# Performance work log

Measured on AMD Instinct MI355X. Metric: run time of the kernel, lower is better.

The kernel has to match this reference:

```python
import jax, jax.numpy as jnp
import numpy as np

B, Q, K, D = 32, 1024, 1024, 128

def setup_inputs() -> dict:
    key = jax.random.key(0)
    kq, kk, kv, kl = jax.random.split(key, 4)
    return {
        "queries": jax.random.normal(kq, (B, Q, D), dtype=jnp.float32),
        "keys": jax.random.normal(kk, (B, K, D), dtype=jnp.float32),
        "values": jax.random.normal(kv, (B, K, D), dtype=jnp.float32),
        "valid_length": jax.random.randint(kl, (B,), 1, K + 1),
    }

def reference(queries, keys, values, valid_length):
    d = queries.shape[-1]
    # scores: [B, Q, K]
    scores = jnp.einsum("bqd,bkd->bqk", queries, keys) / jnp.sqrt(jnp.float32(d))
    # length mask: position k is valid iff k < valid_length[b]
    mask = jnp.arange(keys.shape[1])[None, None, :] < valid_length[:, None, None]
    scores = jnp.where(mask, scores, jnp.float32(-1e9))
    attn = jax.nn.softmax(scores, axis=-1)
    # dropout module is identity in eval / p=0
    return jnp.einsum("bqk,bkv->bqv", attn, values)
```

## Files before the change

kernel.cpp:

```cpp
#include <hip/hip_runtime.h>
#include <hip/hip_bf16.h>
#include <stdint.h>

#define B_    32
#define QLEN  1024
#define KSEQ  1024
#define DIM   128
#define NKT   (KSEQ / 64)
#define SCALE 0.08838834764831845f
#define KSC   0.12751879522655792f

typedef __attribute__((ext_vector_type(8)))  short short8;
typedef __attribute__((ext_vector_type(4)))  float floatx4;
typedef __attribute__((ext_vector_type(16))) float floatx16;
typedef unsigned int u32;

__device__ __forceinline__ u32 f2bf(float x) {
  union { float f; u32 u; } v; v.f = x;
  return (v.u + 0x7FFF + ((v.u >> 16) & 1)) >> 16;
}
__device__ __forceinline__ u32 pack2(float lo, float hi) {
  return f2bf(lo) | (f2bf(hi) << 16);
}
__device__ __forceinline__ u32 cvtpk(float lo, float hi) {
  u32 d;
  asm("v_cvt_pk_bf16_f32 %0, %1, %2" : "=v"(d) : "v"(lo), "v"(hi));
  return d;
}
__device__ __forceinline__ void swap32(u32& a, u32& b) {
  asm volatile("v_permlane32_swap_b32 %0, %1" : "+v"(a), "+v"(b));
}
__device__ __forceinline__ float exp2_fast(float x) {
  float d;
  asm("v_exp_f32 %0, %1" : "=v"(d) : "v"(x));
  return d;
}
typedef union { uint4 u; short8 s; } U8;

__global__ __launch_bounds__(256) void prep_kernel(const float* __restrict__ Kg,
                                                   const float* __restrict__ Vg,
                                                   const int* __restrict__ vlen,
                                                   uint4* __restrict__ Ksw,
                                                   uint4* __restrict__ Vsw,
                                                   int2* __restrict__ task) {
  __shared__ __align__(16) u32 Vu[64 * 65];
  __shared__ __align__(16) uint4 Ku[64 * 17];
  __shared__ int sidx[32];
  const int kt = blockIdx.x, b = blockIdx.y, t = threadIdx.x;
  const bool tableblk = (blockIdx.z == 0) && (kt == 0) && (b == 0);

  if (tableblk && t < 64) {
    const int bb = t & 31;
    const int ntb = (vlen[bb] + 63) >> 6;
    int rank = 0;
#pragma unroll
    for (int j = 0; j < 32; j++) {
      const int ntj = __shfl(ntb, j);
      rank += (ntj > ntb) | ((ntj == ntb) & (j < bb));
    }
    if (t < 32) sidx[rank] = bb;
  }

  if (kt * 64 < vlen[b]) {
    if (blockIdx.z == 0) {
      const float* src = Kg + ((size_t)b * KSEQ + kt * 64) * DIM;
#pragma unroll
      for (int it = 0; it < 4; it++) {
        const int f = it * 256 + t, r = f >> 4, c = f & 15;
        floatx4 f0 = *(const floatx4*)(src + r * DIM + c * 8);
        floatx4 f1 = *(const floatx4*)(src + r * DIM + c * 8 + 4);
        uint4 o;
        o.x = pack2(f0[0] * KSC, f0[1] * KSC); o.y = pack2(f0[2] * KSC, f0[3] * KSC);
        o.z = pack2(f1[0] * KSC, f1[1] * KSC); o.w = pack2(f1[2] * KSC, f1[3] * KSC);
        Ku[r * 17 + c] = o;
      }
      __syncthreads();
      uint4* dst = Ksw + ((size_t)b * NKT + kt) * 1024;
#pragma unroll
      for (int it = 0; it < 4; it++) {
        const int o16 = it * 256 + t;
        const int kh = o16 >> 9, cs = (o16 >> 6) & 7, lane = o16 & 63;
        const int hi = lane >> 5, l31 = lane & 31;
        const int r = kh * 32 + l31, j = 2 * cs + hi;
        dst[o16] = Ku[r * 17 + j];
      }
    } else {
      const float* src = Vg + ((size_t)b * KSEQ + kt * 64) * DIM;
#pragma unroll
      for (int it = 0; it < 8; it++) {
        const int k = it * 8 + (t >> 5), c = t & 31;
        const floatx4 f = *(const floatx4*)(src + (size_t)k * DIM + c * 4);
        const int s = (k >> 3) & 4;
        Vu[k * 65 + ((2 * c) ^ s)]     = pack2(f[0], f[1]);
        Vu[k * 65 + ((2 * c + 1) ^ s)] = pack2(f[2], f[3]);
      }
      __syncthreads();
      uint4* dst = Vsw + ((size_t)b * NKT + kt) * 1024;
#pragma unroll
      for (int it = 0; it < 4; it++) {
        const int o16 = it * 256 + t;
        const int kh = o16 >> 9, slot = (o16 >> 6) & 7, lane = o16 & 63;
        const int dt = slot >> 1, i_ = slot & 1;
        const int hi = lane >> 5, l31 = lane & 31;
        const int d = dt * 32 + l31, m7 = d & 7;
        const int kc = (kh * 4 + 2 * i_ + hi);
        const int col = (d >> 1) ^ (kc & 4);
        u32 r[8];
#pragma unroll
        for (int j = 0; j < 8; j++) r[j] = Vu[(kc * 8 + j) * 65 + col];
        const u32 sel = (d & 1) ? 0x07060302u : 0x05040100u;
        uint4 o;
        o.x = __builtin_amdgcn_perm(r[1], r[0], sel);
        o.y = __builtin_amdgcn_perm(r[3], r[2], sel);
        o.z = __builtin_amdgcn_perm(r[5], r[4], sel);
        o.w = __builtin_amdgcn_perm(r[7], r[6], sel);
        dst[o16] = o;
      }
    }
  }

  if (tableblk) {
    __syncthreads();
    for (int l = t; l < 512; l += 256) {
      const int x = l & 7, j = l >> 3;
      int rank, q;
      if (j < 32) { rank = (j & 1) ? x + 8  : x;      q = j >> 1; }
      else        { rank = (j & 1) ? x + 16 : x + 24; q = (j - 32) >> 1; }
      task[l] = make_int2(sidx[rank], q << 6);
    }
  }
}

__global__ __launch_bounds__(256, 2) void attn_kernel(
    const float* __restrict__ Qg, const uint4* __restrict__ Ksw,
    const uint4* __restrict__ Vsw, const int* __restrict__ vlen,
    const int2* __restrict__ task, float* __restrict__ Og) {
  __shared__ float scr[64 * 128];
  __shared__ float Lred[2][32];

  const int2 tq = task[blockIdx.x];
  const int b = tq.x, q0 = tq.y;
  const int t = threadIdx.x, wave = t >> 6, lane = t & 63;
  const int qh = wave & 1, kh = wave >> 1;
  const int l31 = lane & 31, hi = lane >> 5;
  const int L  = vlen[b];
  const int nt = (L + 63) >> 6;

  const short* KtS = (const short*)(Ksw + (size_t)b * NKT * 1024) +
                     kh * 4096 + lane * 8;
  const short* Vt  = (const short*)(Vsw + (size_t)b * NKT * 1024) +
                     kh * 4096 + lane * 8;

  short8 qb[8];
  {
    const float* qrow = Qg + ((size_t)b * QLEN + q0 + qh * 32 + l31) * DIM;
#pragma unroll
    for (int c = 0; c < 8; c++) {
      floatx4 f0 = *(const floatx4*)(qrow + c * 16 + hi * 8);
      floatx4 f1 = *(const floatx4*)(qrow + c * 16 + hi * 8 + 4);
      short8 a;
      a[0] = (short)f2bf(f0[0]); a[1] = (short)f2bf(f0[1]);
      a[2] = (short)f2bf(f0[2]); a[3] = (short)f2bf(f0[3]);
      a[4] = (short)f2bf(f1[0]); a[5] = (short)f2bf(f1[1]);
      a[6] = (short)f2bf(f1[2]); a[7] = (short)f2bf(f1[3]);
      qb[c] = a;
    }
  }

  float lrow = 0.0f;
  floatx16 oacc[4];
#pragma unroll
  for (int dt = 0; dt < 4; dt++)
#pragma unroll
    for (int i = 0; i < 16; i++) oacc[dt][i] = 0.0f;

#define LOAD_K(DST, tkv)                                                       \
  {                                                                            \
    const short* kp_ = KtS + (size_t)(tkv) * 8192;                             \
    _Pragma("unroll") for (int c_ = 0; c_ < 8; c_++)                           \
      DST[c_] = *(const short8*)(kp_ + c_ * 512);                              \
  }

#define BODY(KF, tkv)                                                          \
  {                                                                            \
    const int k0_ = (tkv) * 64;                                                \
    short8 vb[4][2];                                                           \
    {                                                                          \
      const short* vt_ = Vt + (size_t)(tkv) * 8192;                            \
      _Pragma("unroll") for (int dt = 0; dt < 4; dt++) {                       \
        vb[dt][0] = *(const short8*)(vt_ + (dt * 2 + 0) * 512);                \
        vb[dt][1] = *(const short8*)(vt_ + (dt * 2 + 1) * 512);                \
      }                                                                        \
    }                                                                          \
    floatx16 s;                                                                \
    _Pragma("unroll") for (int i = 0; i < 16; i++) s[i] = 0.0f;                \
    __builtin_amdgcn_s_setprio(1);                                             \
    _Pragma("unroll") for (int c = 0; c < 8; c++)                              \
      s = __builtin_amdgcn_mfma_f32_32x32x16_bf16(KF[c], qb[c], s, 0, 0, 0);   \
    __builtin_amdgcn_s_setprio(0);                                             \
    if (k0_ + kh * 32 + 32 <= L) {                                             \
      _Pragma("unroll") for (int r = 0; r < 16; r++) {                         \
        s[r] = exp2_fast(s[r]);                                                \
        lrow += s[r];                                                          \
      }                                                                        \
    } else {                                                                   \
      _Pragma("unroll") for (int r = 0; r < 16; r++) {                         \
        const int ck = (r & 3) + 8 * (r >> 2) + 4 * hi;                        \
        const float a = (k0_ + kh * 32 + ck < L) ? exp2_fast(s[r]) : 0.0f;     \
        s[r] = a;                                                              \
        lrow += a;                                                             \
      }                                                                        \
    }                                                                          \
    {                                                                          \
      u32 u0 = cvtpk(s[0], s[1]),   u1 = cvtpk(s[2], s[3]);                    \
      u32 u2 = cvtpk(s[4], s[5]),   u3 = cvtpk(s[6], s[7]);                    \
      swap32(u0, u2); swap32(u1, u3);                                          \
      u32 w0 = cvtpk(s[8], s[9]),   w1 = cvtpk(s[10], s[11]);                  \
      u32 w2 = cvtpk(s[12], s[13]), w3 = cvtpk(s[14], s[15]);                  \
      swap32(w0, w2); swap32(w1, w3);                                          \
      U8 pu0; pu0.u.x = u0; pu0.u.y = u1; pu0.u.z = u2; pu0.u.w = u3;          \
      U8 pu1; pu1.u.x = w0; pu1.u.y = w1; pu1.u.z = w2; pu1.u.w = w3;          \
      __builtin_amdgcn_s_setprio(1);                                           \
      _Pragma("unroll") for (int dt = 0; dt < 4; dt++) {                       \
        oacc[dt] = __builtin_amdgcn_mfma_f32_32x32x16_bf16(pu0.s, vb[dt][0],   \
                                                           oacc[dt], 0, 0, 0);\
        oacc[dt] = __builtin_amdgcn_mfma_f32_32x32x16_bf16(pu1.s, vb[dt][1],   \
                                                           oacc[dt], 0, 0, 0);\
      }                                                                        \
      __builtin_amdgcn_s_setprio(0);                                           \
    }                                                                          \
  }

  short8 ka[8], kb[8];
  LOAD_K(ka, 0);
  int tk = 0;
  for (;;) {
    if (tk + 1 < nt) LOAD_K(kb, tk + 1);
    BODY(ka, tk);
    if (++tk == nt) break;
    if (tk + 1 < nt) LOAD_K(ka, tk + 1);
    BODY(kb, tk);
    if (++tk == nt) break;
  }

  lrow += __shfl_xor(lrow, 32);
  if (kh == 1) {
    if (lane < 32) Lred[qh][l31] = lrow;
#pragma unroll
    for (int dt = 0; dt < 4; dt++)
#pragma unroll
      for (int r = 0; r < 16; r++)
        scr[(dt * 16 + r) * 128 + qh * 64 + lane] = oacc[dt][r];
  }
  __syncthreads();
  if (kh == 0) {
    const float ltot = lrow + Lred[qh][l31];
    const float inv_ = 1.0f / ltot;
    float iv[16];
#pragma unroll
    for (int r = 0; r < 16; r++)
      iv[r] = __shfl(inv_, (r & 3) + 8 * (r >> 2) + 4 * hi);
    float* obase = Og + ((size_t)b * QLEN + q0 + qh * 32) * DIM + l31;
#pragma unroll
    for (int dt = 0; dt < 4; dt++) {
#pragma unroll
      for (int r = 0; r < 16; r++) {
        const int rq = (r & 3) + 8 * (r >> 2) + 4 * hi;
        const float v = oacc[dt][r] + scr[(dt * 16 + r) * 128 + qh * 64 + lane];
        obase[(size_t)rq * DIM + dt * 32] = v * iv[r];
      }
    }
  }
#undef LOAD_K
#undef BODY
}

extern "C" void kernel_launch(void* const* d_in, const int* in_sizes, int n_in,
                              void* d_out, int out_size, void* d_ws, size_t ws_size,
                              hipStream_t stream) {
  const float* Qg = (const float*)d_in[0];
  const float* Kg = (const float*)d_in[1];
  const float* Vg = (const float*)d_in[2];
  const int*  vln = (const int*)d_in[3];
  uint4* Ksw = (uint4*)d_ws;
  uint4* Vsw = (uint4*)((char*)d_ws + (size_t)B_ * NKT * 16384);
  int2*  Tsk = (int2*)((char*)d_ws + 2 * (size_t)B_ * NKT * 16384);

  prep_kernel<<<dim3(NKT, B_, 2), 256, 0, stream>>>(Kg, Vg, vln, Ksw, Vsw, Tsk);
  attn_kernel<<<dim3(512), 256, 0, stream>>>(Qg, Ksw, Vsw, vln, Tsk,
                                             (float*)d_out);
}
```

Baseline: 110.8 us.

## Software-pipeline QK^T of next tile with softmax and PV of current tile

Restructures the main loop so the QK^T MFMAs for tile k+1 are issued before the exp/convert/PV work of tile k, using two score accumulators (sA/sB) and a single K fragment buffer loaded two tiles ahead. The aim is to overlap matrix-core work with the transcendental and pack VALU work, and to hide K/V load latency. The row-sum is also turned into a tree reduction. The cost is extra register pressure from a second live 16-float score tile, which could lower occupancy or cause spills.

```diff
diff --git a/kernel.cpp b/kernel.cpp
--- a/kernel.cpp
+++ b/kernel.cpp
@@ -7,7 +7,6 @@
 #define KSEQ  1024
 #define DIM   128
 #define NKT   (KSEQ / 64)
-#define SCALE 0.08838834764831845f
 #define KSC   0.12751879522655792f
 
 typedef __attribute__((ext_vector_type(8)))  short short8;
@@ -102,7 +101,7 @@
         const int kh = o16 >> 9, slot = (o16 >> 6) & 7, lane = o16 & 63;
         const int dt = slot >> 1, i_ = slot & 1;
         const int hi = lane >> 5, l31 = lane & 31;
-        const int d = dt * 32 + l31, m7 = d & 7;
+        const int d = dt * 32 + l31;
         const int kc = (kh * 4 + 2 * i_ + hi);
         const int col = (d >> 1) ^ (kc & 4);
         u32 r[8];
@@ -174,72 +173,80 @@
 #pragma unroll
     for (int i = 0; i < 16; i++) oacc[dt][i] = 0.0f;
 
-#define LOAD_K(DST, tkv)                                                       \
+  short8 kf[8];
+  short8 vb[4][2];
+  floatx16 sA, sB;
+
+#define LOAD_K(tkv)                                                            \
   {                                                                            \
     const short* kp_ = KtS + (size_t)(tkv) * 8192;                             \
     _Pragma("unroll") for (int c_ = 0; c_ < 8; c_++)                           \
-      DST[c_] = *(const short8*)(kp_ + c_ * 512);                              \
-  }
-
-#define BODY(KF, tkv)                                                          \
+      kf[c_] = *(const short8*)(kp_ + c_ * 512);                               \
+  }
+
+#define LOAD_V(tkv)                                                            \
+  {                                                                            \
+    const short* vt_ = Vt + (size_t)(tkv) * 8192;                              \
+    _Pragma("unroll") for (int dt = 0; dt < 4; dt++) {                         \
+      vb[dt][0] = *(const short8*)(vt_ + (dt * 2 + 0) * 512);                  \
+      vb[dt][1] = *(const short8*)(vt_ + (dt * 2 + 1) * 512);                  \
+    }                                                                          \
+  }
+
+#define QKT(SD)                                                                \
+  {                                                                            \
+    _Pragma("unroll") for (int i = 0; i < 16; i++) SD[i] = 0.0f;               \
+    _Pragma("unroll") for (int c = 0; c < 8; c++)                              \
+      SD = __builtin_amdgcn_mfma_f32_32x32x16_bf16(kf[c], qb[c], SD, 0, 0, 0); \
+  }
+
+#define SMPV(SV, tkv)                                                          \
   {                                                                            \
     const int k0_ = (tkv) * 64;                                                \
-    short8 vb[4][2];                                                           \
-    {                                                                          \
-      const short* vt_ = Vt + (size_t)(tkv) * 8192;                            \
-      _Pragma("unroll") for (int dt = 0; dt < 4; dt++) {                       \
-        vb[dt][0] = *(const short8*)(vt_ + (dt * 2 + 0) * 512);                \
-        vb[dt][1] = *(const short8*)(vt_ + (dt * 2 + 1) * 512);                \
-      }                                                                        \
-    }                                                                          \
-    floatx16 s;                                                                \
-    _Pragma("unroll") for (int i = 0; i < 16; i++) s[i] = 0.0f;                \
-    __builtin_amdgcn_s_setprio(1);                                             \
-    _Pragma("unroll") for (int c = 0; c < 8; c++)                              \
-      s = __builtin_amdgcn_mfma_f32_32x32x16_bf16(KF[c], qb[c], s, 0, 0, 0);   \
-    __builtin_amdgcn_s_setprio(0);                                             \
     if (k0_ + kh * 32 + 32 <= L) {                                             \
-      _Pragma("unroll") for (int r = 0; r < 16; r++) {                         \
-        s[r] = exp2_fast(s[r]);                                                \
-        lrow += s[r];                                                          \
-      }                                                                        \
+      _Pragma("unroll") for (int r = 0; r < 16; r++) SV[r] = exp2_fast(SV[r]); \
     } else {                                                                   \
       _Pragma("unroll") for (int r = 0; r < 16; r++) {                         \
         const int ck = (r & 3) + 8 * (r >> 2) + 4 * hi;                        \
-        const float a = (k0_ + kh * 32 + ck < L) ? exp2_fast(s[r]) : 0.0f;     \
-        s[r] = a;                                                              \
-        lrow += a;                                                             \
+        SV[r] = (k0_ + kh * 32 + ck < L) ? exp2_fast(SV[r]) : 0.0f;            \
       }                                                                        \
     }                                                                          \
-    {                                                                          \
-      u32 u0 = cvtpk(s[0], s[1]),   u1 = cvtpk(s[2], s[3]);                    \
-      u32 u2 = cvtpk(s[4], s[5]),   u3 = cvtpk(s[6], s[7]);                    \
-      swap32(u0, u2); swap32(u1, u3);                                          \
-      u32 w0 = cvtpk(s[8], s[9]),   w1 = cvtpk(s[10], s[11]);                  \
-      u32 w2 = cvtpk(s[12], s[13]), w3 = cvtpk(s[14], s[15]);                  \
-      swap32(w0, w2); swap32(w1, w3);                                          \
-      U8 pu0; pu0.u.x = u0; pu0.u.y = u1; pu0.u.z = u2; pu0.u.w = u3;          \
-      U8 pu1; pu1.u.x = w0; pu1.u.y = w1; pu1.u.z = w2; pu1.u.w = w3;          \
-      __builtin_amdgcn_s_setprio(1);                                           \
-      _Pragma("unroll") for (int dt = 0; dt < 4; dt++) {                       \
-        oacc[dt] = __builtin_amdgcn_mfma_f32_32x32x16_bf16(pu0.s, vb[dt][0],   \
-                                                           oacc[dt], 0, 0, 0);\
-        oacc[dt] = __builtin_amdgcn_mfma_f32_32x32x16_bf16(pu1.s, vb[dt][1],   \
-                                                           oacc[dt], 0, 0, 0);\
-      }                                                                        \
-      __builtin_amdgcn_s_setprio(0);                                           \
+    lrow += (((SV[0] + SV[1]) + (SV[2] + SV[3])) +                             \
+             ((SV[4] + SV[5]) + (SV[6] + SV[7]))) +                            \
+            (((SV[8] + SV[9]) + (SV[10] + SV[11])) +                           \
+             ((SV[12] + SV[13]) + (SV[14] + SV[15])));                         \
+    u32 u0 = cvtpk(SV[0], SV[1]),   u1 = cvtpk(SV[2], SV[3]);                  \
+    u32 u2 = cvtpk(SV[4], SV[5]),   u3 = cvtpk(SV[6], SV[7]);                  \
+    swap32(u0, u2); swap32(u1, u3);                                            \
+    u32 w0 = cvtpk(SV[8], SV[9]),   w1 = cvtpk(SV[10], SV[11]);                \
+    u32 w2 = cvtpk(SV[12], SV[13]), w3 = cvtpk(SV[14], SV[15]);                \
+    swap32(w0, w2); swap32(w1, w3);                                            \
+    U8 pu0; pu0.u.x = u0; pu0.u.y = u1; pu0.u.z = u2; pu0.u.w = u3;            \
+    U8 pu1; pu1.u.x = w0; pu1.u.y = w1; pu1.u.z = w2; pu1.u.w = w3;            \
+    __builtin_amdgcn_s_setprio(1);                                             \
+    _Pragma("unroll") for (int dt = 0; dt < 4; dt++) {                         \
+      oacc[dt] = __builtin_amdgcn_mfma_f32_32x32x16_bf16(pu0.s, vb[dt][0],     \
+                                                         oacc[dt], 0, 0, 0);   \
+      oacc[dt] = __builtin_amdgcn_mfma_f32_32x32x16_bf16(pu1.s, vb[dt][1],     \
+                                                         oacc[dt], 0, 0, 0);   \
     }                                                                          \
-  }
-
-  short8 ka[8], kb[8];
-  LOAD_K(ka, 0);
+    __builtin_amdgcn_s_setprio(0);                                             \
+  }
+
+  LOAD_K(0);
+  QKT(sA);
+  if (nt > 1) LOAD_K(1);
   int tk = 0;
   for (;;) {
-    if (tk + 1 < nt) LOAD_K(kb, tk + 1);
-    BODY(ka, tk);
+    LOAD_V(tk);
+    if (tk + 1 < nt) QKT(sB);
+    if (tk + 2 < nt) LOAD_K(tk + 2);
+    SMPV(sA, tk);
     if (++tk == nt) break;
-    if (tk + 1 < nt) LOAD_K(ka, tk + 1);
-    BODY(kb, tk);
+    LOAD_V(tk);
+    if (tk + 1 < nt) QKT(sA);
+    if (tk + 2 < nt) LOAD_K(tk + 2);
+    SMPV(sB, tk);
     if (++tk == nt) break;
   }
 
@@ -272,7 +279,9 @@
     }
   }
 #undef LOAD_K
-#undef BODY
+#undef LOAD_V
+#undef QKT
+#undef SMPV
 }
 
 extern "C" void kernel_launch(void* const* d_in, const int* in_sizes, int n_in,
```

Result: no change. 111.9 us (+1.0%).
